# Kernel tuning notes

Hardware: AMD Instinct MI355X
Metric: run time of the kernel (lower is better)

The kernel has to match this reference:

```python
import jax, jax.numpy as jnp
import numpy as np

H = 32               # num_heads
NUM_EDGES = 1536
NUM_SPATIAL = 512
NUM_EDGE_DIS = 128
MHMD = 5             # multi_hop_max_dist


def setup_inputs() -> dict:
    key = jax.random.key(0)
    ks = jax.random.split(key, 9)
    B, N = 32, 128
    std = 0.02
    attn_bias = jax.random.normal(ks[0], (B, N + 1, N + 1), jnp.float32)
    spatial_pos = jax.random.randint(ks[1], (B, N, N), 0, NUM_SPATIAL)
    x = jax.random.randint(ks[2], (B, N, 1), 0, 512)
    edge_input = jax.random.randint(ks[3], (B, N, N, MHMD, 3), 0, NUM_EDGES + 1)
    attn_edge_type = jax.random.randint(ks[4], (B, N, N, 3), 0, NUM_EDGES + 1)
    # embedding tables (padding_idx=0 rows zeroed, matching nn.Embedding padding_idx)
    edge_encoder_w = (jax.random.normal(ks[5], (NUM_EDGES + 1, H), jnp.float32) * std).at[0].set(0.0)
    spatial_pos_encoder_w = (jax.random.normal(ks[6], (NUM_SPATIAL, H), jnp.float32) * std).at[0].set(0.0)
    edge_dis_encoder_w = jax.random.normal(ks[7], (NUM_EDGE_DIS * H * H, 1), jnp.float32) * std
    graph_token_virtual_distance_w = jax.random.normal(ks[8], (1, H), jnp.float32) * std
    return {
        'attn_bias': attn_bias,
        'spatial_pos': spatial_pos,
        'x': x,
        'edge_input': edge_input,
        'attn_edge_type': attn_edge_type,
        'edge_encoder_w': edge_encoder_w,
        'edge_dis_encoder_w': edge_dis_encoder_w,
        'spatial_pos_encoder_w': spatial_pos_encoder_w,
        'graph_token_virtual_distance_w': graph_token_virtual_distance_w,
    }


def reference(attn_bias, spatial_pos, x, edge_input, attn_edge_type,
              edge_encoder_w, edge_dis_encoder_w, spatial_pos_encoder_w,
              graph_token_virtual_distance_w):
    B, Np1, _ = attn_bias.shape
    # [B, H, n+1, n+1] base bias replicated per head
    g = jnp.broadcast_to(attn_bias[:, None, :, :], (B, H, Np1, Np1))
    # spatial (SPD) bias: gather -> [B, n, n, H] -> [B, H, n, n]
    spb = spatial_pos_encoder_w[spatial_pos].transpose(0, 3, 1, 2)
    g = g.at[:, :, 1:, 1:].add(spb)
    # virtual distance to graph token
    t = graph_token_virtual_distance_w.reshape(1, H, 1)
    g = g.at[:, :, 1:, 0].add(t)
    g = g.at[:, :, 0, :].add(t)
    # multi-hop edge encoding
    sp = jnp.where(spatial_pos == 0, 1, spatial_pos)
    sp = jnp.where(sp > 1, sp - 1, sp)
    sp = jnp.clip(sp, 0, MHMD)
    # gather edge embeddings, mean over edge-feature dim: [B,n,n,D,H]
    ei = edge_encoder_w[edge_input[..., :MHMD, :]].mean(axis=-2)
    D = ei.shape[-2]
    Wd = edge_dis_encoder_w.reshape(NUM_EDGE_DIS, H, H)[:D]
    # tiny per-distance HxH matmul
    ei = jnp.einsum('bijdh,dhk->bijdk', ei, Wd)
    ei = ei.sum(axis=-2) / sp.astype(ei.dtype)[..., None]   # [B,n,n,H]
    g = g.at[:, :, 1:, 1:].add(ei.transpose(0, 3, 1, 2))
    # residual add of raw attn_bias
    g = g + attn_bias[:, None, :, :]
    return g
```

## Files before the change

### kernel.cpp

```cpp
#include <hip/hip_runtime.h>
#include <hip/hip_bf16.h>

#define BB 32
#define NN 128
#define HH 32
#define NP1 129
#define NE1 1537
#define MHMD 5
#define HG 4
#define NHG (HH / HG)


__global__ __launch_bounds__(256) void precompute_Mt(const float* __restrict__ E,
                                                     const float* __restrict__ W,
                                                     __hip_bfloat16* __restrict__ Mt) {
    int idx = blockIdx.x * 256 + threadIdx.x;
    if (idx >= MHMD * NE1 * HH) return;
    int k = idx & 31;
    int r = (idx >> 5) % NE1;
    int d = idx / (NE1 * HH);
    const float* wd = W + d * HH * HH;
    float acc = 0.f;
#pragma unroll
    for (int h = 0; h < HH; ++h)
        acc += E[r * HH + h] * wd[h * HH + k];
    int hg = k >> 2, hl = k & 3;
    Mt[(((size_t)hg * MHMD + d) * NE1 + r) * HG + hl] = __float2bfloat16(acc);
}

__global__ __launch_bounds__(256) void precompute_spwT(const float* __restrict__ spw,
                                                       float* __restrict__ spwT) {
    int idx = blockIdx.x * 256 + threadIdx.x;
    if (idx >= 512 * HH) return;
    int k = idx & 31, s = idx >> 5;
    spwT[(((k >> 2) * 512) + s) * HG + (k & 3)] = spw[idx];
}

__global__ __launch_bounds__(256) void border_kernel(const float* __restrict__ ab,
                                                     const float* __restrict__ tvd,
                                                     float* __restrict__ out) {
    int idx = blockIdx.x * 256 + threadIdx.x;
    if (idx >= BB * HH * 257) return;
    int pos = idx % 257;
    int bh  = idx / 257;
    int h = bh & 31, b = bh >> 5;
    int r, c;
    if (pos < NP1) { r = 0; c = pos; }
    else           { r = pos - 128; c = 0; }
    float v = 2.0f * ab[((size_t)b * NP1 + r) * NP1 + c] + tvd[h];
    out[(((size_t)b * HH + h) * NP1 + r) * NP1 + c] = v;
}

__global__ __launch_bounds__(1024) void inner_kernel(const float* __restrict__ ab,
                                                     const int* __restrict__ spatial,
                                                     const int* __restrict__ edge_input,
                                                     const __hip_bfloat16* __restrict__ Mt,
                                                     const float* __restrict__ spwT,
                                                     float* __restrict__ out) {
    __shared__ uint2  sM[MHMD * NE1];
    __shared__ float4 sS[512];

    const int bid   = blockIdx.x;
    const int b     = bid & 31;
    const int hg    = (bid >> 5) & 7;
    const int ihalf = bid >> 8;
    const int t     = threadIdx.x;

    const uint* msrc = (const uint*)(Mt + (size_t)hg * MHMD * NE1 * HG);
    uint* mdst = (uint*)sM;
    for (int x = t; x < (MHMD * NE1 * HG) / 2; x += 1024)
        mdst[x] = msrc[x];
    const float4* ssrc = (const float4*)(spwT + (size_t)hg * 512 * HG);
    if (t < 512) sS[t] = ssrc[t];
    __syncthreads();

    const int*   eb   = edge_input + (size_t)b * NN * NN * 15;
    const int*   spb  = spatial    + (size_t)b * NN * NN;
    const float* abb  = ab         + (size_t)b * NP1 * NP1;
    float*       outb = out + ((size_t)(b * HH + hg * HG)) * NP1 * NP1;
    const size_t PL = (size_t)NP1 * NP1;

#pragma unroll
    for (int c = 0; c < 8; ++c) {
        int cell = ihalf * 8192 + c * 1024 + t;
        int i = cell >> 7, j = cell & 127;
        const int* ep = eb + (size_t)cell * 15;
        int e[15];
#pragma unroll
        for (int p = 0; p < 15; ++p) e[p] = ep[p];

        float a0 = 0.f, a1 = 0.f, a2 = 0.f, a3 = 0.f;
#pragma unroll
        for (int p = 0; p < 15; ++p) {
            uint2 v = sM[(p / 3) * NE1 + e[p]];
            a0 += __uint_as_float(v.x << 16);
            a1 += __uint_as_float(v.x & 0xffff0000u);
            a2 += __uint_as_float(v.y << 16);
            a3 += __uint_as_float(v.y & 0xffff0000u);
        }
        int sp  = spb[cell];
        int sp1 = sp <= 1 ? 1 : min(sp - 1, MHMD);
        float m = __builtin_amdgcn_rcpf(3.0f * (float)sp1);
        float4 sw = sS[sp];
        float av  = 2.0f * abb[(i + 1) * NP1 + (j + 1)];
        size_t o  = (size_t)(i + 1) * NP1 + (j + 1);
        outb[o]          = av + sw.x + a0 * m;
        outb[o + PL]     = av + sw.y + a1 * m;
        outb[o + 2 * PL] = av + sw.z + a2 * m;
        outb[o + 3 * PL] = av + sw.w + a3 * m;
    }
}

__global__ __launch_bounds__(256) void inner_direct(const float* __restrict__ ab,
                                                    const int* __restrict__ spatial,
                                                    const int* __restrict__ edge_input,
                                                    const float* __restrict__ E,
                                                    const float* __restrict__ W,
                                                    const float* __restrict__ spw,
                                                    float* __restrict__ out) {
    long idx = (long)blockIdx.x * 256 + threadIdx.x;
    if (idx >= (long)BB * NN * NN * HH) return;
    int h = idx & 31;
    long cell = idx >> 5;
    int j  = cell & 127;
    int bi = (int)(cell >> 7);
    int i  = bi & 127;
    int b  = bi >> 7;
    const int* e = edge_input + cell * 15;
    float acc = 0.f;
    for (int d = 0; d < MHMD; ++d) {
        const float* wd = W + d * HH * HH;
        int e0 = e[d * 3 + 0] * HH, e1 = e[d * 3 + 1] * HH, e2 = e[d * 3 + 2] * HH;
        for (int hp = 0; hp < HH; ++hp) {
            float eh = E[e0 + hp] + E[e1 + hp] + E[e2 + hp];
            acc += eh * wd[hp * HH + h];
        }
    }
    int spd = spatial[cell];
    int sp1 = spd == 0 ? 1 : spd;
    sp1 = sp1 > 1 ? sp1 - 1 : sp1;
    sp1 = sp1 > MHMD ? MHMD : sp1;
    float v = spw[spd * HH + h] + acc / (3.0f * (float)sp1);
    out[(((size_t)b * HH + h) * NP1 + (i + 1)) * NP1 + (j + 1)] =
        2.0f * ab[((size_t)b * NP1 + (i + 1)) * NP1 + (j + 1)] + v;
}

extern "C" void kernel_launch(void* const* d_in, const int* in_sizes, int n_in,
                              void* d_out, int out_size, void* d_ws, size_t ws_size,
                              hipStream_t stream) {
    const float* ab      = (const float*)d_in[0];
    const int*   spatial = (const int*)  d_in[1];
    const int*   edge_in = (const int*)  d_in[3];
    const float* E       = (const float*)d_in[5];
    const float* W       = (const float*)d_in[6];
    const float* spw     = (const float*)d_in[7];
    const float* tvd     = (const float*)d_in[8];
    float* out = (float*)d_out;

    border_kernel<<<(BB * HH * 257 + 255) / 256, 256, 0, stream>>>(ab, tvd, out);

    const size_t Mt_bytes  = (size_t)NHG * MHMD * NE1 * HG * sizeof(__hip_bfloat16);
    const size_t spw_bytes = (size_t)NHG * 512 * HG * sizeof(float);
    if (ws_size >= Mt_bytes + spw_bytes) {
        __hip_bfloat16* Mt  = (__hip_bfloat16*)d_ws;
        float*          spT = (float*)((char*)d_ws + Mt_bytes);
        precompute_Mt<<<(MHMD * NE1 * HH + 255) / 256, 256, 0, stream>>>(E, W, Mt);
        precompute_spwT<<<(512 * HH + 255) / 256, 256, 0, stream>>>(spw, spT);
        inner_kernel<<<512, 1024, 0, stream>>>(ab, spatial, edge_in, Mt, spT, out);
    } else {
        long total = (long)BB * NN * NN * HH;
        inner_direct<<<(unsigned)((total + 255) / 256), 256, 0, stream>>>(
            ab, spatial, edge_in, E, W, spw, out);
    }
}
```

Measured before the change: 161.7 us.

## Stage edge indices through LDS with coalesced int4 loads and register prefetch

Each thread used to read its 15 edge indices with a 60-byte-strided gather from global memory. The inner kernel now loads each chunk of edge indices with coalesced int4 loads into a shared-memory buffer, and prefetches the next chunk into registers while the current one is being processed. The LDS gathers are also batched ahead of the accumulation. In exchange, the extra ~60KB of shared memory raises per-block LDS use to about 130KB, which likely allows only one block per CU, and adds two barriers per chunk.

```diff
diff --git a/kernel.cpp b/kernel.cpp
--- a/kernel.cpp
+++ b/kernel.cpp
@@ -59,6 +59,7 @@
                                                      float* __restrict__ out) {
     __shared__ uint2  sM[MHMD * NE1];
     __shared__ float4 sS[512];
+    __shared__ int    sE[1024 * 15];
 
     const int bid   = blockIdx.x;
     const int b     = bid & 31;
@@ -72,42 +73,72 @@
         mdst[x] = msrc[x];
     const float4* ssrc = (const float4*)(spwT + (size_t)hg * 512 * HG);
     if (t < 512) sS[t] = ssrc[t];
-    __syncthreads();
-
-    const int*   eb   = edge_input + (size_t)b * NN * NN * 15;
-    const int*   spb  = spatial    + (size_t)b * NN * NN;
-    const float* abb  = ab         + (size_t)b * NP1 * NP1;
+
+    const int*   spb  = spatial + (size_t)b * NN * NN;
+    const float* abb  = ab      + (size_t)b * NP1 * NP1;
     float*       outb = out + ((size_t)(b * HH + hg * HG)) * NP1 * NP1;
     const size_t PL = (size_t)NP1 * NP1;
 
-#pragma unroll
-    for (int c = 0; c < 8; ++c) {
-        int cell = ihalf * 8192 + c * 1024 + t;
-        int i = cell >> 7, j = cell & 127;
-        const int* ep = eb + (size_t)cell * 15;
+    const int4* esrc = (const int4*)(edge_input
+                     + (size_t)b * NN * NN * 15 + (size_t)ihalf * 8192 * 15);
+
+    int4 pf0, pf1, pf2, pf3;
+    {
+        pf0 = esrc[t];
+        pf1 = esrc[1024 + t];
+        pf2 = esrc[2048 + t];
+        pf3 = (3072 + t < 3840) ? esrc[3072 + t] : make_int4(0, 0, 0, 0);
+    }
+
+    for (int ch = 0; ch < 8; ++ch) {
+        int4* ed = (int4*)sE;
+        ed[t]        = pf0;
+        ed[1024 + t] = pf1;
+        ed[2048 + t] = pf2;
+        if (3072 + t < 3840) ed[3072 + t] = pf3;
+        __syncthreads();
+
+        if (ch < 7) {
+            const int4* nsrc = esrc + (ch + 1) * 3840;
+            pf0 = nsrc[t];
+            pf1 = nsrc[1024 + t];
+            pf2 = nsrc[2048 + t];
+            pf3 = (3072 + t < 3840) ? nsrc[3072 + t] : make_int4(0, 0, 0, 0);
+        }
+
+        const int cell = ihalf * 8192 + ch * 1024 + t;
+        const int i = cell >> 7, j = cell & 127;
+
+        const int   sp = spb[cell];
+        const float av = 2.0f * abb[(i + 1) * NP1 + (j + 1)];
+
         int e[15];
 #pragma unroll
-        for (int p = 0; p < 15; ++p) e[p] = ep[p];
+        for (int p = 0; p < 15; ++p) e[p] = sE[t * 15 + p];
+
+        uint2 v[15];
+#pragma unroll
+        for (int p = 0; p < 15; ++p)
+            v[p] = sM[(p / 3) * NE1 + e[p]];
 
         float a0 = 0.f, a1 = 0.f, a2 = 0.f, a3 = 0.f;
 #pragma unroll
         for (int p = 0; p < 15; ++p) {
-            uint2 v = sM[(p / 3) * NE1 + e[p]];
-            a0 += __uint_as_float(v.x << 16);
-            a1 += __uint_as_float(v.x & 0xffff0000u);
-            a2 += __uint_as_float(v.y << 16);
-            a3 += __uint_as_float(v.y & 0xffff0000u);
+            a0 += __uint_as_float(v[p].x << 16);
+            a1 += __uint_as_float(v[p].x & 0xffff0000u);
+            a2 += __uint_as_float(v[p].y << 16);
+            a3 += __uint_as_float(v[p].y & 0xffff0000u);
         }
-        int sp  = spb[cell];
-        int sp1 = sp <= 1 ? 1 : min(sp - 1, MHMD);
-        float m = __builtin_amdgcn_rcpf(3.0f * (float)sp1);
-        float4 sw = sS[sp];
-        float av  = 2.0f * abb[(i + 1) * NP1 + (j + 1)];
-        size_t o  = (size_t)(i + 1) * NP1 + (j + 1);
+        const int sp1 = sp <= 1 ? 1 : min(sp - 1, MHMD);
+        const float m = __builtin_amdgcn_rcpf(3.0f * (float)sp1);
+        const float4 sw = sS[sp];
+
+        const size_t o = (size_t)(i + 1) * NP1 + (j + 1);
         outb[o]          = av + sw.x + a0 * m;
         outb[o + PL]     = av + sw.y + a1 * m;
         outb[o + 2 * PL] = av + sw.z + a2 * m;
         outb[o + 3 * PL] = av + sw.w + a3 * m;
+        __syncthreads();
     }
 }
 
```

Measured after the change: 158.7 us. No clear change (-1.9%).
